# Performance work log

Measured on AMD Instinct MI355X. Metric: run time of the kernel, lower is better.

Reference implementation:

```python
import jax, jax.numpy as jnp
import numpy as np

N_EDGES = 65536
D = 512          # n_hidden
H = 8            # num_heads
DH = D // H      # head_dim
LN_EPS = 1e-5


def _layernorm(x, g, b):
    m = jnp.mean(x, axis=-1, keepdims=True)
    v = jnp.mean(jnp.square(x - m), axis=-1, keepdims=True)
    return (x - m) * jax.lax.rsqrt(v + LN_EPS) * g + b


def setup_inputs() -> dict:
    key = jax.random.key(0)
    ks = jax.random.split(key, 10)
    s = 1.0 / np.sqrt(D)      # ~kaiming-uniform scale for nn.Linear
    s4 = 1.0 / np.sqrt(4 * D)
    return {
        "query_input": jax.random.normal(ks[0], (N_EDGES, D), jnp.float32),
        "source_input": jax.random.normal(ks[1], (N_EDGES, D), jnp.float32),
        "Wq": jax.random.normal(ks[2], (D, D), jnp.float32) * s,
        "bq": jnp.zeros((D,), jnp.float32),
        "Wk": jax.random.normal(ks[3], (D, D), jnp.float32) * s,
        "bk": jnp.zeros((D,), jnp.float32),
        "Wv": jax.random.normal(ks[4], (D, D), jnp.float32) * s,
        "bv": jnp.zeros((D,), jnp.float32),
        "Wh": jax.random.normal(ks[5], (D, D), jnp.float32) * s,
        "bh": jnp.zeros((D,), jnp.float32),
        "ln_kv_g": jnp.ones((D,), jnp.float32),
        "ln_kv_b": jnp.zeros((D,), jnp.float32),
        "ln_q_g": jnp.ones((D,), jnp.float32),
        "ln_q_b": jnp.zeros((D,), jnp.float32),
        "ln2_g": jnp.ones((D,), jnp.float32),
        "ln2_b": jnp.zeros((D,), jnp.float32),
        "W1": jax.random.normal(ks[6], (D, 4 * D), jnp.float32) * s,
        "b1": jnp.zeros((4 * D,), jnp.float32),
        "W2": jax.random.normal(ks[7], (4 * D, D), jnp.float32) * s4,
        "b2": jnp.zeros((D,), jnp.float32),
    }


def reference(query_input, source_input, Wq, bq, Wk, bk, Wv, bv, Wh, bh,
              ln_kv_g, ln_kv_b, ln_q_g, ln_q_b, ln2_g, ln2_b,
              W1, b1, W2, b2):
    n = query_input.shape[0]
    ln_src = _layernorm(source_input, ln_kv_g, ln_kv_b)
    ln_qry = _layernorm(query_input, ln_q_g, ln_q_b)

    qs = (ln_qry @ Wq + bq).reshape(n, H, DH)
    ks = (ln_src @ Wk + bk).reshape(n, H, DH)
    vs = (ln_src @ Wv + bv).reshape(n, H, DH)

    # torch.norm(qs, p=2) with no dim => GLOBAL Frobenius norm (faithful to source)
    qs = qs / jnp.linalg.norm(qs)
    ks = ks / jnp.linalg.norm(ks)

    nf = jnp.asarray(n, qs.dtype)
    kvs = jnp.einsum('nhd,nhk->hdk', ks, vs)                 # [H, DH, DH]
    # 'nhd,hdd->nhd' : repeated d on kvs takes its DIAGONAL (torch semantics)
    attention_num = jnp.einsum('nhd,hdd->nhd', qs, kvs) + vs * nf
    ks_sum = jnp.sum(ks, axis=0)                             # == einsum('nhd,n->hd', ks, ones)
    normalizer = jnp.einsum('nhd,hd->nh', qs, ks_sum)[..., None] + nf
    attn_output = (attention_num / normalizer).reshape(n, H * DH)

    h_post_attention = attn_output @ Wh + bh
    h_pre_ffn = source_input + h_post_attention              # dropout = identity (eval)
    y = _layernorm(h_pre_ffn, ln2_g, ln2_b)
    h_post_ffn = jax.nn.gelu(y @ W1 + b1, approximate=False) @ W2 + b2
    return h_pre_ffn + h_post_ffn
```

## Files before the change

kernel.cpp:

```cpp
#include <hip/hip_runtime.h>
#include <hip/hip_bf16.h>

#define NROWS 65536
#define LN_EPS 1e-5f

typedef __attribute__((ext_vector_type(8))) short bf16x8;
typedef __attribute__((ext_vector_type(4))) float f32x4;

__device__ __forceinline__ float bf2f(unsigned short u) {
  union { unsigned u; float f; } c; c.u = ((unsigned)u) << 16; return c.f;
}
__device__ __forceinline__ unsigned short f2bf(float f) {
  union { float f; unsigned u; } c; c.f = f;
  return (unsigned short)((c.u + 0x7fffu + ((c.u >> 16) & 1u)) >> 16);
}

__launch_bounds__(256)
__global__ void normcast_k(const float* __restrict__ x, unsigned short* __restrict__ o) {
  int t = threadIdx.x;
  int row = blockIdx.x * 4 + (t >> 6);
  int lane = t & 63;
  const float* p = x + (size_t)row * 512 + lane * 8;
  float4 a = *(const float4*)p;
  float4 b = *(const float4*)(p + 4);
  float s = a.x + a.y + a.z + a.w + b.x + b.y + b.z + b.w;
  float q = a.x*a.x + a.y*a.y + a.z*a.z + a.w*a.w
          + b.x*b.x + b.y*b.y + b.z*b.z + b.w*b.w;
#pragma unroll
  for (int off = 1; off < 64; off <<= 1) {
    s += __shfl_xor(s, off);
    q += __shfl_xor(q, off);
  }
  float mean = s * (1.0f / 512.0f);
  float r = rsqrtf(q * (1.0f / 512.0f) - mean * mean + LN_EPS);
  float va[8] = {a.x, a.y, a.z, a.w, b.x, b.y, b.z, b.w};
  unsigned pk[4];
#pragma unroll
  for (int i = 0; i < 4; ++i) {
    unsigned lo = f2bf((va[2 * i] - mean) * r);
    unsigned hi = f2bf((va[2 * i + 1] - mean) * r);
    pk[i] = lo | (hi << 16);
  }
  uint4 u; u.x = pk[0]; u.y = pk[1]; u.z = pk[2]; u.w = pk[3];
  *(uint4*)(o + (size_t)row * 512 + lane * 8) = u;
}

__launch_bounds__(256)
__global__ void transbf_k(const float* __restrict__ W, const float* __restrict__ g,
                          unsigned short* __restrict__ Wt, int K, int N) {
  __shared__ float tile[32][33];
  int tx = threadIdx.x & 31, ty = threadIdx.x >> 5;
  int n0 = blockIdx.x * 32, k0 = blockIdx.y * 32;
#pragma unroll
  for (int i = 0; i < 4; ++i) {
    int k = k0 + ty + i * 8;
    float gg = g ? g[k] : 1.0f;
    tile[ty + i * 8][tx] = gg * W[(size_t)k * N + n0 + tx];
  }
  __syncthreads();
#pragma unroll
  for (int i = 0; i < 4; ++i) {
    int n = n0 + ty + i * 8;
    Wt[(size_t)n * K + k0 + tx] = f2bf(tile[tx][ty + i * 8]);
  }
}

__launch_bounds__(256)
__global__ void betacalc_k(const float* __restrict__ W, const float* __restrict__ b,
                           const float* __restrict__ bias, float* __restrict__ beta,
                           int K, int N) {
  int n = blockIdx.x * 256 + threadIdx.x;
  float s = 0.f;
  for (int k = 0; k < K; ++k) s += b[k] * W[(size_t)k * N + n];
  beta[n] = s + bias[n];
}

#define M_Q  0
#define M_KV 1
#define M_H  3
#define M_F1 4
#define M_F2 5

template <int MODE>
__launch_bounds__(256)
__global__ void mm_k(const unsigned short* __restrict__ A,
                     const unsigned short* __restrict__ Bt,
                     void* __restrict__ Ov,
                     const float* __restrict__ beta,
                     const float* __restrict__ src,
                     float* __restrict__ scal,
                     int N, int K) {
  __shared__ __align__(16) unsigned short As[128 * 64];
  __shared__ __align__(16) unsigned short Bs[128 * 64];
  __shared__ float red[4];
  const int t = threadIdx.x;
  const int lane = t & 63;
  const int wave = t >> 6;

  const unsigned gx = gridDim.x;
  unsigned bid = blockIdx.y * gx + blockIdx.x;
  const unsigned cpx = (gx * gridDim.y) >> 3;
  bid = (bid & 7u) * cpx + (bid >> 3);
  const int m0 = (int)(bid / gx) * 128;
  const int n0 = (int)(bid % gx) * 128;

  const int srow = lane >> 3;
  const int sxor = ((lane & 7) ^ srow) * 8;
  const int wm = (wave >> 1) * 64;
  const int wn = (wave & 1) * 64;
  const int quad = lane >> 4;
  const int l15 = lane & 15;
  const int l7 = lane & 7;

  f32x4 acc[4][4];
#pragma unroll
  for (int i = 0; i < 4; ++i)
#pragma unroll
    for (int j = 0; j < 4; ++j) acc[i][j] = (f32x4){0.f, 0.f, 0.f, 0.f};

  for (int k0 = 0; k0 < K; k0 += 64) {
    __syncthreads();
#pragma unroll
    for (int i = 0; i < 4; ++i) {
      int c = wave * 4 + i;
      int grow = c * 8 + srow;
      const unsigned short* ga = A + (size_t)(m0 + grow) * K + k0 + sxor;
      const unsigned short* gb = Bt + (size_t)(n0 + grow) * K + k0 + sxor;
      __builtin_amdgcn_global_load_lds(
          (const __attribute__((address_space(1))) void*)ga,
          (__attribute__((address_space(3))) void*)(As + c * 512), 16, 0, 0);
      __builtin_amdgcn_global_load_lds(
          (const __attribute__((address_space(1))) void*)gb,
          (__attribute__((address_space(3))) void*)(Bs + c * 512), 16, 0, 0);
    }
    __syncthreads();
#pragma unroll
    for (int kt = 0; kt < 2; ++kt) {
      const int pb = ((kt * 4 + quad) ^ l7) * 8;
      bf16x8 af[4], bfr[4];
#pragma unroll
      for (int x = 0; x < 4; ++x) {
        af[x]  = *(const bf16x8*)(As + (wm + x * 16 + l15) * 64 + pb);
        bfr[x] = *(const bf16x8*)(Bs + (wn + x * 16 + l15) * 64 + pb);
      }
#pragma unroll
      for (int mi = 0; mi < 4; ++mi)
#pragma unroll
        for (int nj = 0; nj < 4; ++nj)
          acc[mi][nj] = __builtin_amdgcn_mfma_f32_16x16x32_bf16(
              af[mi], bfr[nj], acc[mi][nj], 0, 0, 0);
    }
  }

  float lred = 0.f;
#pragma unroll
  for (int mi = 0; mi < 4; ++mi) {
#pragma unroll
    for (int nj = 0; nj < 4; ++nj) {
      const int col = n0 + wn + nj * 16 + l15;
      const float bet = beta[col];
      size_t idx = (size_t)(m0 + wm + mi * 16 + quad * 4) * N + col;
#pragma unroll
      for (int r = 0; r < 4; ++r, idx += N) {
        float v = acc[mi][nj][r] + bet;
        if constexpr (MODE == M_Q || MODE == M_KV) {
          lred += v * v;
          ((unsigned short*)Ov)[idx] = f2bf(v);
        } else if constexpr (MODE == M_H) {
          ((float*)Ov)[idx] = v + src[idx];
        } else if constexpr (MODE == M_F1) {
          float t2 = v * v;
          float y2 = 1.5957691216f * v * __builtin_fmaf(0.044715f, t2, 1.0f);
          float e = __expf(y2);
          float rr = __builtin_amdgcn_rcpf(e + 1.0f);
          float gl = v - v * rr;
          ((unsigned short*)Ov)[idx] = f2bf(gl);
        } else {
          ((float*)Ov)[idx] += v;
        }
      }
    }
  }
  if constexpr (MODE == M_Q || MODE == M_KV) {
    if (MODE == M_Q || n0 < 512) {
#pragma unroll
      for (int off = 32; off > 0; off >>= 1) lred += __shfl_xor(lred, off);
      if (lane == 0) red[wave] = lred;
      __syncthreads();
      if (t == 0) atomicAdd(scal, red[0] + red[1] + red[2] + red[3]);
    }
  }
}

__launch_bounds__(256)
__global__ void colred_k(const unsigned short* __restrict__ KV,
                         float* __restrict__ S1, float* __restrict__ S2) {
  int t = threadIdx.x;
  int c0 = t * 2;
  int r0 = blockIdx.x * 128;
  float s1a = 0.f, s1b = 0.f, s2a = 0.f, s2b = 0.f;
  for (int r = 0; r < 128; ++r) {
    const unsigned short* base = KV + (size_t)(r0 + r) * 1024;
    unsigned ku = *(const unsigned*)(base + c0);
    unsigned vu = *(const unsigned*)(base + 512 + c0);
    float k0 = bf2f((unsigned short)(ku & 0xffff));
    float k1 = bf2f((unsigned short)(ku >> 16));
    float v0 = bf2f((unsigned short)(vu & 0xffff));
    float v1 = bf2f((unsigned short)(vu >> 16));
    s1a += k0 * v0; s1b += k1 * v1;
    s2a += k0;      s2b += k1;
  }
  atomicAdd(&S1[c0], s1a); atomicAdd(&S1[c0 + 1], s1b);
  atomicAdd(&S2[c0], s2a); atomicAdd(&S2[c0 + 1], s2b);
}

__launch_bounds__(256)
__global__ void attn_k(unsigned short* __restrict__ Qb, const unsigned short* __restrict__ KV,
                       const float* __restrict__ S1, const float* __restrict__ S2,
                       const float* __restrict__ sqq, const float* __restrict__ skk) {
  int t = threadIdx.x;
  int row = blockIdx.x * 4 + (t >> 6);
  int lane = t & 63;
  int c = lane * 8;
  float inv = rsqrtf(sqq[0] * skk[0]);
  const float Nf = (float)NROWS;
  unsigned short* qp = Qb + (size_t)row * 512 + c;
  uint4 qu = *(const uint4*)qp;
  float q[8];
  q[0] = bf2f((unsigned short)(qu.x & 0xffff)); q[1] = bf2f((unsigned short)(qu.x >> 16));
  q[2] = bf2f((unsigned short)(qu.y & 0xffff)); q[3] = bf2f((unsigned short)(qu.y >> 16));
  q[4] = bf2f((unsigned short)(qu.z & 0xffff)); q[5] = bf2f((unsigned short)(qu.z >> 16));
  q[6] = bf2f((unsigned short)(qu.w & 0xffff)); q[7] = bf2f((unsigned short)(qu.w >> 16));
  const unsigned short* vp = KV + (size_t)row * 1024 + 512 + c;
  uint4 vu = *(const uint4*)vp;
  float vv[8];
  vv[0] = bf2f((unsigned short)(vu.x & 0xffff)); vv[1] = bf2f((unsigned short)(vu.x >> 16));
  vv[2] = bf2f((unsigned short)(vu.y & 0xffff)); vv[3] = bf2f((unsigned short)(vu.y >> 16));
  vv[4] = bf2f((unsigned short)(vu.z & 0xffff)); vv[5] = bf2f((unsigned short)(vu.z >> 16));
  vv[6] = bf2f((unsigned short)(vu.w & 0xffff)); vv[7] = bf2f((unsigned short)(vu.w >> 16));
  float4 s10 = *(const float4*)(S1 + c), s11 = *(const float4*)(S1 + c + 4);
  float4 s20 = *(const float4*)(S2 + c), s21 = *(const float4*)(S2 + c + 4);
  float s1v[8] = {s10.x, s10.y, s10.z, s10.w, s11.x, s11.y, s11.z, s11.w};
  float s2v[8] = {s20.x, s20.y, s20.z, s20.w, s21.x, s21.y, s21.z, s21.w};
  float part = 0.f;
#pragma unroll
  for (int i = 0; i < 8; ++i) part += q[i] * s2v[i];
  part += __shfl_xor(part, 1);
  part += __shfl_xor(part, 2);
  part += __shfl_xor(part, 4);
  float rn = 1.0f / (inv * part + Nf);
  unsigned pk[4];
#pragma unroll
  for (int i = 0; i < 4; ++i) {
    float o0 = (q[2 * i] * s1v[2 * i] * inv + vv[2 * i] * Nf) * rn;
    float o1 = (q[2 * i + 1] * s1v[2 * i + 1] * inv + vv[2 * i + 1] * Nf) * rn;
    pk[i] = (unsigned)f2bf(o0) | ((unsigned)f2bf(o1) << 16);
  }
  uint4 u; u.x = pk[0]; u.y = pk[1]; u.z = pk[2]; u.w = pk[3];
  *(uint4*)qp = u;
}

extern "C" void kernel_launch(void* const* d_in, const int* in_sizes, int n_in,
                              void* d_out, int out_size, void* d_ws, size_t ws_size,
                              hipStream_t stream) {
  const float* query   = (const float*)d_in[0];
  const float* source  = (const float*)d_in[1];
  const float* Wq      = (const float*)d_in[2];
  const float* bq      = (const float*)d_in[3];
  const float* Wk      = (const float*)d_in[4];
  const float* bk      = (const float*)d_in[5];
  const float* Wv      = (const float*)d_in[6];
  const float* bv      = (const float*)d_in[7];
  const float* Wh      = (const float*)d_in[8];
  const float* bh      = (const float*)d_in[9];
  const float* ln_kv_g = (const float*)d_in[10];
  const float* ln_kv_b = (const float*)d_in[11];
  const float* ln_q_g  = (const float*)d_in[12];
  const float* ln_q_b  = (const float*)d_in[13];
  const float* ln2_g   = (const float*)d_in[14];
  const float* ln2_b   = (const float*)d_in[15];
  const float* W1      = (const float*)d_in[16];
  const float* b1      = (const float*)d_in[17];
  const float* W2      = (const float*)d_in[18];
  const float* b2      = (const float*)d_in[19];
  float* out = (float*)d_out;

  const size_t MB = 1024 * 1024;
  char* w = (char*)d_ws;
  unsigned short* Qn = (unsigned short*)(w + 0 * MB);
  unsigned short* Sn = (unsigned short*)(w + 64 * MB);
  unsigned short* Qb = (unsigned short*)(w + 128 * MB);
  unsigned short* KV = (unsigned short*)(w + 192 * MB);
  unsigned short* Hn = (unsigned short*)(w + 320 * MB);
  unsigned short* Tb = (unsigned short*)(w + 0 * MB);
  char* wt = w + 384 * MB;
  unsigned short* Wqt = (unsigned short*)wt;
  unsigned short* Wkt = Wqt + 512 * 512;
  unsigned short* Wvt = Wkt + 512 * 512;
  unsigned short* Wht = Wvt + 512 * 512;
  unsigned short* W1t = Wht + 512 * 512;
  unsigned short* W2t = W1t + 512 * 2048;
  float* betaq = (float*)(W2t + 2048 * 512);
  float* betak = betaq + 512;
  float* betav = betak + 512;
  float* betaf = betav + 512;
  float* S1 = betaf + 2048;
  float* S2 = S1 + 512;
  float* SQQ = S2 + 512;
  float* SKK = SQQ + 1;

  hipMemsetAsync(S1, 0, (512 + 512 + 2) * sizeof(float), stream);

  dim3 blk(256);
  normcast_k<<<NROWS / 4, blk, 0, stream>>>(query, Qn);
  normcast_k<<<NROWS / 4, blk, 0, stream>>>(source, Sn);
  transbf_k<<<dim3(16, 16), blk, 0, stream>>>(Wq, ln_q_g, Wqt, 512, 512);
  transbf_k<<<dim3(16, 16), blk, 0, stream>>>(Wk, ln_kv_g, Wkt, 512, 512);
  transbf_k<<<dim3(16, 16), blk, 0, stream>>>(Wv, ln_kv_g, Wvt, 512, 512);
  transbf_k<<<dim3(16, 16), blk, 0, stream>>>(Wh, nullptr, Wht, 512, 512);
  transbf_k<<<dim3(64, 16), blk, 0, stream>>>(W1, ln2_g, W1t, 512, 2048);
  transbf_k<<<dim3(16, 64), blk, 0, stream>>>(W2, nullptr, W2t, 2048, 512);
  betacalc_k<<<2, blk, 0, stream>>>(Wq, ln_q_b, bq, betaq, 512, 512);
  betacalc_k<<<2, blk, 0, stream>>>(Wk, ln_kv_b, bk, betak, 512, 512);
  betacalc_k<<<2, blk, 0, stream>>>(Wv, ln_kv_b, bv, betav, 512, 512);
  betacalc_k<<<8, blk, 0, stream>>>(W1, ln2_b, b1, betaf, 512, 2048);

  dim3 g512(4, 512);
  mm_k<M_Q><<<g512, blk, 0, stream>>>(Qn, Wqt, Qb, betaq, nullptr, SQQ, 512, 512);
  mm_k<M_KV><<<dim3(8, 512), blk, 0, stream>>>(Sn, Wkt, KV, betak, nullptr, SKK, 1024, 512);
  colred_k<<<NROWS / 128, blk, 0, stream>>>(KV, S1, S2);
  attn_k<<<NROWS / 4, blk, 0, stream>>>(Qb, KV, S1, S2, SQQ, SKK);
  mm_k<M_H><<<g512, blk, 0, stream>>>(Qb, Wht, out, bh, source, nullptr, 512, 512);
  normcast_k<<<NROWS / 4, blk, 0, stream>>>(out, Hn);
  dim3 g2048(16, 512);
  mm_k<M_F1><<<g2048, blk, 0, stream>>>(Hn, W1t, Tb, betaf, nullptr, nullptr, 2048, 512);
  mm_k<M_F2><<<g512, blk, 0, stream>>>(Tb, W2t, out, b2, nullptr, nullptr, 512, 2048);
}
```

Baseline: 1.770 ms.

## Fuse K·V column reductions into KV GEMM epilogue and drop K buffer

The KV projection GEMM now interleaves K and V columns so each tile holds matching 64-column slices of K and V. The epilogue stages V in shared memory, computes the per-column sums of K·V and of K in-register, and adds them atomically into S1/S2. This removes the separate colred kernel and the write and re-read of the full K matrix, so only V is stored. In exchange the GEMM gets a longer epilogue with extra syncs, LDS traffic and atomics, and the sums are now taken over fp32 values rather than bf16-rounded ones.

```diff
diff --git a/kernel.cpp b/kernel.cpp
--- a/kernel.cpp
+++ b/kernel.cpp
@@ -89,10 +89,13 @@
                      const float* __restrict__ beta,
                      const float* __restrict__ src,
                      float* __restrict__ scal,
+                     float* __restrict__ S1,
+                     float* __restrict__ S2,
                      int N, int K) {
-  __shared__ __align__(16) unsigned short As[128 * 64];
-  __shared__ __align__(16) unsigned short Bs[128 * 64];
+  __shared__ __align__(16) unsigned short AsBs[2 * 128 * 64];
   __shared__ float red[4];
+  unsigned short* As = AsBs;
+  unsigned short* Bs = AsBs + 128 * 64;
   const int t = threadIdx.x;
   const int lane = t & 63;
   const int wave = t >> 6;
@@ -103,6 +106,7 @@
   bid = (bid & 7u) * cpx + (bid >> 3);
   const int m0 = (int)(bid / gx) * 128;
   const int n0 = (int)(bid % gx) * 128;
+  const int g64 = n0 >> 1;
 
   const int srow = lane >> 3;
   const int sxor = ((lane & 7) ^ srow) * 8;
@@ -125,7 +129,13 @@
       int c = wave * 4 + i;
       int grow = c * 8 + srow;
       const unsigned short* ga = A + (size_t)(m0 + grow) * K + k0 + sxor;
-      const unsigned short* gb = Bt + (size_t)(n0 + grow) * K + k0 + sxor;
+      const unsigned short* gb;
+      if constexpr (MODE == M_KV) {
+        int btrow = (c < 8) ? (g64 + grow) : (512 - 64 + g64 + grow);
+        gb = Bt + (size_t)btrow * K + k0 + sxor;
+      } else {
+        gb = Bt + (size_t)(n0 + grow) * K + k0 + sxor;
+      }
       __builtin_amdgcn_global_load_lds(
           (const __attribute__((address_space(1))) void*)ga,
           (__attribute__((address_space(3))) void*)(As + c * 512), 16, 0, 0);
@@ -153,69 +163,102 @@
   }
 
   float lred = 0.f;
-#pragma unroll
-  for (int mi = 0; mi < 4; ++mi) {
-#pragma unroll
-    for (int nj = 0; nj < 4; ++nj) {
-      const int col = n0 + wn + nj * 16 + l15;
-      const float bet = beta[col];
-      size_t idx = (size_t)(m0 + wm + mi * 16 + quad * 4) * N + col;
-#pragma unroll
-      for (int r = 0; r < 4; ++r, idx += N) {
-        float v = acc[mi][nj][r] + bet;
-        if constexpr (MODE == M_Q || MODE == M_KV) {
-          lred += v * v;
-          ((unsigned short*)Ov)[idx] = f2bf(v);
-        } else if constexpr (MODE == M_H) {
-          ((float*)Ov)[idx] = v + src[idx];
-        } else if constexpr (MODE == M_F1) {
-          float t2 = v * v;
-          float y2 = 1.5957691216f * v * __builtin_fmaf(0.044715f, t2, 1.0f);
-          float e = __expf(y2);
-          float rr = __builtin_amdgcn_rcpf(e + 1.0f);
-          float gl = v - v * rr;
-          ((unsigned short*)Ov)[idx] = f2bf(gl);
-        } else {
-          ((float*)Ov)[idx] += v;
+  if constexpr (MODE == M_KV) {
+    float* Vx = (float*)AsBs;
+    __syncthreads();
+    if (wn) {
+#pragma unroll
+      for (int mi = 0; mi < 4; ++mi) {
+#pragma unroll
+        for (int nj = 0; nj < 4; ++nj) {
+          const int colv = nj * 16 + l15;
+          const float bet = beta[512 + g64 + colv];
+          size_t idx = (size_t)(m0 + wm + mi * 16 + quad * 4) * 512 + g64 + colv;
+#pragma unroll
+          for (int r = 0; r < 4; ++r, idx += 512) {
+            float v = acc[mi][nj][r] + bet;
+            int lr = wm + mi * 16 + quad * 4 + r;
+            Vx[lr * 64 + (colv ^ (((lr >> 2) & 3) << 4))] = v;
+            ((unsigned short*)Ov)[idx] = f2bf(v);
+          }
         }
       }
     }
+    __syncthreads();
+    if (!wn) {
+      float s1[4] = {0.f, 0.f, 0.f, 0.f};
+      float s2[4] = {0.f, 0.f, 0.f, 0.f};
+#pragma unroll
+      for (int mi = 0; mi < 4; ++mi) {
+#pragma unroll
+        for (int nj = 0; nj < 4; ++nj) {
+          const int colv = nj * 16 + l15;
+          const float bet = beta[g64 + colv];
+#pragma unroll
+          for (int r = 0; r < 4; ++r) {
+            float v = acc[mi][nj][r] + bet;
+            lred += v * v;
+            int lr = wm + mi * 16 + quad * 4 + r;
+            float vv = Vx[lr * 64 + (colv ^ (((lr >> 2) & 3) << 4))];
+            s1[nj] += v * vv;
+            s2[nj] += v;
+          }
+        }
+      }
+#pragma unroll
+      for (int nj = 0; nj < 4; ++nj) {
+        s1[nj] += __shfl_xor(s1[nj], 16); s1[nj] += __shfl_xor(s1[nj], 32);
+        s2[nj] += __shfl_xor(s2[nj], 16); s2[nj] += __shfl_xor(s2[nj], 32);
+      }
+      if (quad == 0) {
+#pragma unroll
+        for (int nj = 0; nj < 4; ++nj) {
+          atomicAdd(&S1[g64 + nj * 16 + l15], s1[nj]);
+          atomicAdd(&S2[g64 + nj * 16 + l15], s2[nj]);
+        }
+      }
+    }
+  } else {
+#pragma unroll
+    for (int mi = 0; mi < 4; ++mi) {
+#pragma unroll
+      for (int nj = 0; nj < 4; ++nj) {
+        const int col = n0 + wn + nj * 16 + l15;
+        const float bet = beta[col];
+        size_t idx = (size_t)(m0 + wm + mi * 16 + quad * 4) * N + col;
+#pragma unroll
+        for (int r = 0; r < 4; ++r, idx += N) {
+          float v = acc[mi][nj][r] + bet;
+          if constexpr (MODE == M_Q) {
+            lred += v * v;
+            ((unsigned short*)Ov)[idx] = f2bf(v);
+          } else if constexpr (MODE == M_H) {
+            ((float*)Ov)[idx] = v + src[idx];
+          } else if constexpr (MODE == M_F1) {
+            float t2 = v * v;
+            float y2 = 1.5957691216f * v * __builtin_fmaf(0.044715f, t2, 1.0f);
+            float e = __expf(y2);
+            float rr = __builtin_amdgcn_rcpf(e + 1.0f);
+            float gl = v - v * rr;
+            ((unsigned short*)Ov)[idx] = f2bf(gl);
+          } else {
+            ((float*)Ov)[idx] += v;
+          }
+        }
+      }
+    }
   }
   if constexpr (MODE == M_Q || MODE == M_KV) {
-    if (MODE == M_Q || n0 < 512) {
-#pragma unroll
-      for (int off = 32; off > 0; off >>= 1) lred += __shfl_xor(lred, off);
-      if (lane == 0) red[wave] = lred;
-      __syncthreads();
-      if (t == 0) atomicAdd(scal, red[0] + red[1] + red[2] + red[3]);
-    }
-  }
-}
-
-__launch_bounds__(256)
-__global__ void colred_k(const unsigned short* __restrict__ KV,
-                         float* __restrict__ S1, float* __restrict__ S2) {
-  int t = threadIdx.x;
-  int c0 = t * 2;
-  int r0 = blockIdx.x * 128;
-  float s1a = 0.f, s1b = 0.f, s2a = 0.f, s2b = 0.f;
-  for (int r = 0; r < 128; ++r) {
-    const unsigned short* base = KV + (size_t)(r0 + r) * 1024;
-    unsigned ku = *(const unsigned*)(base + c0);
-    unsigned vu = *(const unsigned*)(base + 512 + c0);
-    float k0 = bf2f((unsigned short)(ku & 0xffff));
-    float k1 = bf2f((unsigned short)(ku >> 16));
-    float v0 = bf2f((unsigned short)(vu & 0xffff));
-    float v1 = bf2f((unsigned short)(vu >> 16));
-    s1a += k0 * v0; s1b += k1 * v1;
-    s2a += k0;      s2b += k1;
-  }
-  atomicAdd(&S1[c0], s1a); atomicAdd(&S1[c0 + 1], s1b);
-  atomicAdd(&S2[c0], s2a); atomicAdd(&S2[c0 + 1], s2b);
-}
-
-__launch_bounds__(256)
-__global__ void attn_k(unsigned short* __restrict__ Qb, const unsigned short* __restrict__ KV,
+#pragma unroll
+    for (int off = 32; off > 0; off >>= 1) lred += __shfl_xor(lred, off);
+    if (lane == 0) red[wave] = lred;
+    __syncthreads();
+    if (t == 0) atomicAdd(scal, red[0] + red[1] + red[2] + red[3]);
+  }
+}
+
+__launch_bounds__(256)
+__global__ void attn_k(unsigned short* __restrict__ Qb, const unsigned short* __restrict__ Vb,
                        const float* __restrict__ S1, const float* __restrict__ S2,
                        const float* __restrict__ sqq, const float* __restrict__ skk) {
   int t = threadIdx.x;
@@ -231,7 +274,7 @@
   q[2] = bf2f((unsigned short)(qu.y & 0xffff)); q[3] = bf2f((unsigned short)(qu.y >> 16));
   q[4] = bf2f((unsigned short)(qu.z & 0xffff)); q[5] = bf2f((unsigned short)(qu.z >> 16));
   q[6] = bf2f((unsigned short)(qu.w & 0xffff)); q[7] = bf2f((unsigned short)(qu.w >> 16));
-  const unsigned short* vp = KV + (size_t)row * 1024 + 512 + c;
+  const unsigned short* vp = Vb + (size_t)row * 512 + c;
   uint4 vu = *(const uint4*)vp;
   float vv[8];
   vv[0] = bf2f((unsigned short)(vu.x & 0xffff)); vv[1] = bf2f((unsigned short)(vu.x >> 16));
@@ -290,8 +333,8 @@
   unsigned short* Qn = (unsigned short*)(w + 0 * MB);
   unsigned short* Sn = (unsigned short*)(w + 64 * MB);
   unsigned short* Qb = (unsigned short*)(w + 128 * MB);
-  unsigned short* KV = (unsigned short*)(w + 192 * MB);
-  unsigned short* Hn = (unsigned short*)(w + 320 * MB);
+  unsigned short* Vb = (unsigned short*)(w + 192 * MB);
+  unsigned short* Hn = (unsigned short*)(w + 256 * MB);
   unsigned short* Tb = (unsigned short*)(w + 0 * MB);
   char* wt = w + 384 * MB;
   unsigned short* Wqt = (unsigned short*)wt;
@@ -326,13 +369,12 @@
   betacalc_k<<<8, blk, 0, stream>>>(W1, ln2_b, b1, betaf, 512, 2048);
 
   dim3 g512(4, 512);
-  mm_k<M_Q><<<g512, blk, 0, stream>>>(Qn, Wqt, Qb, betaq, nullptr, SQQ, 512, 512);
-  mm_k<M_KV><<<dim3(8, 512), blk, 0, stream>>>(Sn, Wkt, KV, betak, nullptr, SKK, 1024, 512);
-  colred_k<<<NROWS / 128, blk, 0, stream>>>(KV, S1, S2);
-  attn_k<<<NROWS / 4, blk, 0, stream>>>(Qb, KV, S1, S2, SQQ, SKK);
-  mm_k<M_H><<<g512, blk, 0, stream>>>(Qb, Wht, out, bh, source, nullptr, 512, 512);
+  mm_k<M_Q><<<g512, blk, 0, stream>>>(Qn, Wqt, Qb, betaq, nullptr, SQQ, nullptr, nullptr, 512, 512);
+  mm_k<M_KV><<<dim3(8, 512), blk, 0, stream>>>(Sn, Wkt, Vb, betak, nullptr, SKK, S1, S2, 512, 512);
+  attn_k<<<NROWS / 4, blk, 0, stream>>>(Qb, Vb, S1, S2, SQQ, SKK);
+  mm_k<M_H><<<g512, blk, 0, stream>>>(Qb, Wht, out, bh, source, nullptr, nullptr, nullptr, 512, 512);
   normcast_k<<<NROWS / 4, blk, 0, stream>>>(out, Hn);
   dim3 g2048(16, 512);
-  mm_k<M_F1><<<g2048, blk, 0, stream>>>(Hn, W1t, Tb, betaf, nullptr, nullptr, 2048, 512);
-  mm_k<M_F2><<<g512, blk, 0, stream>>>(Tb, W2t, out, b2, nullptr, nullptr, 512, 2048);
-}
+  mm_k<M_F1><<<g2048, blk, 0, stream>>>(Hn, W1t, Tb, betaf, nullptr, nullptr, nullptr, nullptr, 2048, 512);
+  mm_k<M_F2><<<g512, blk, 0, stream>>>(Tb, W2t, out, b2, nullptr, nullptr, nullptr, nullptr, 512, 2048);
+}
```

Measured after the change: 1.728 ms. 2.4% less time.
